# Kernel optimization log

Measured on AMD Instinct MI355X. Metric: run time of the kernel, lower is better.

## Reference

```python
import jax, jax.numpy as jnp
import numpy as np

MARGIN = 0.2  # matches init_kwargs; margin > 0 -> relu hinge branch

N_PARTS, NUM_CLASSES, K_PER_CLASS, D_FEAT = 64, 32, 16, 256


def setup_inputs() -> dict:
    key = jax.random.key(0)
    m = NUM_CLASSES * K_PER_CLASS  # 512
    feature = jax.random.normal(key, (N_PARTS, m, D_FEAT), dtype=jnp.float32)
    # Structured P x K labels: masked_select(...).view(n, m, -1, 1) in the
    # original requires exactly K positives per anchor, so labels must be
    # K samples per class (identical across the part dimension).
    label = jnp.tile(jnp.repeat(jnp.arange(NUM_CLASSES, dtype=jnp.int64), K_PER_CLASS)[None, :], (N_PARTS, 1))
    return {"feature": feature, "label": label, "num_pos": K_PER_CLASS}


def _batch_euc_dist(x):
    # x: [n, m, d] -> dist: [n, m, m]
    x2 = jnp.sum(x * x, axis=2)  # [n, m]
    d2 = x2[:, :, None] + x2[:, None, :] - 2.0 * jnp.einsum('nid,njd->nij', x, x)
    return jnp.sqrt(jax.nn.relu(d2))


def reference(feature, label, num_pos):
    n, m, d = feature.shape
    dist = _batch_euc_dist(feature)  # [n, m, m]
    same = label[:, :, None] == label[:, None, :]  # [n, m, m] bool
    # masked_select preserves flat (row-major) order, so per anchor the
    # selected positives/negatives appear in increasing index order ->
    # stable argsort on the mask reproduces it exactly.
    pos_idx = jnp.argsort(jnp.where(same, 0, 1), axis=-1)[..., :num_pos]        # [n, m, k]
    neg_idx = jnp.argsort(jnp.where(same, 1, 0), axis=-1)[..., :m - num_pos]    # [n, m, m-k]
    hp = jnp.take_along_axis(dist, pos_idx, axis=-1)[:, :, :, None]   # [n, m, k, 1]
    hn = jnp.take_along_axis(dist, neg_idx, axis=-1)[:, :, None, :]   # [n, m, 1, m-k]
    # margin > 0 -> relu hinge (heter/hard/part mining disabled by init flags)
    loss = jax.nn.relu(MARGIN + hp - hn).reshape(n, -1)               # [n, m*k*(m-k)]
    nonzero_num = jnp.sum(loss != 0, axis=1).astype(loss.dtype)       # [n]
    loss_mean = jnp.where(nonzero_num == 0, 0.0,
                          jnp.sum(loss, axis=1) / jnp.maximum(nonzero_num, 1.0))
    return loss_mean.mean(), nonzero_num.mean()
```

## Files before the change

### kernel.cpp

```cpp
#include <hip/hip_runtime.h>
#include <math.h>


#define MARGIN 0.2f
constexpr int NP = 64;
constexpr int M = 512;
constexpr int D = 256;
constexpr int SDS = 20;

typedef __attribute__((ext_vector_type(8))) short bf16x8;
typedef __attribute__((ext_vector_type(4))) float f32x4;

__device__ __forceinline__ unsigned f2bf(float x) {
  unsigned b = __float_as_uint(x);
  return (b + 0x7FFFu + ((b >> 16) & 1u)) >> 16;
}
__device__ __forceinline__ uint4 pack8(float4 v0, float4 v1) {
  uint4 p;
  p.x = f2bf(v0.x) | (f2bf(v0.y) << 16);
  p.y = f2bf(v0.z) | (f2bf(v0.w) << 16);
  p.z = f2bf(v1.x) | (f2bf(v1.y) << 16);
  p.w = f2bf(v1.z) | (f2bf(v1.w) << 16);
  return p;
}

__global__ __launch_bounds__(256, 2) void triplet_kernel(
    const float* __restrict__ feat, float* __restrict__ psum,
    float* __restrict__ pcnt) {
  __shared__ unsigned short As[64 * 32 * 8];
  __shared__ unsigned short Bs[64 * 16 * 8];
  __shared__ float sortd[64 * SDS];
  __shared__ float sumt[64 * SDS];
  __shared__ float x2s[M];
  __shared__ float reds[4], redc[4];

  const int p = blockIdx.y;
  const int diag = blockIdx.x;
  const int i0 = diag * 64;
  const int t = threadIdx.x;
  const int w = t >> 6;
  const int L = t & 63;
  const int tx = L & 15, quad = L >> 4;

  const float* fp = feat + (size_t)p * M * D;

#pragma unroll
  for (int r8 = 0; r8 < 8; r8++) {
    const int row = (t >> 5) + r8 * 8;
    const int c = t & 31;
    const float* src = fp + (size_t)(i0 + row) * D + c * 8;
    float4 v0 = ((const float4*)src)[0];
    float4 v1 = ((const float4*)src)[1];
    *(uint4*)&As[(row * 32 + (c ^ (row & 7))) * 8] = pack8(v0, v1);
  }

  float x2i[4];
  f32x4 srt[4][4];
  float hsum = 0.f;
  int hcnt = 0;

  for (int tt = 0; tt < 8; tt++) {
    const int jt = (diag + tt) & 7;
    const int j0 = jt * 64;
    f32x4 acc[4];
#pragma unroll
    for (int f = 0; f < 4; f++) acc[f] = (f32x4){0.f, 0.f, 0.f, 0.f};
    float rowss[4] = {0.f, 0.f, 0.f, 0.f};

#pragma unroll
    for (int kc = 0; kc < 2; kc++) {
      __syncthreads();
#pragma unroll
      for (int r4 = 0; r4 < 4; r4++) {
        const int row = (t >> 4) + r4 * 16;
        const int c = t & 15;
        const float* src = fp + (size_t)(j0 + row) * D + kc * 128 + c * 8;
        float4 v0 = ((const float4*)src)[0];
        float4 v1 = ((const float4*)src)[1];
        *(uint4*)&Bs[(row * 16 + (c ^ (row & 7))) * 8] = pack8(v0, v1);
        rowss[r4] += v0.x * v0.x + v0.y * v0.y + v0.z * v0.z + v0.w * v0.w +
                     v1.x * v1.x + v1.y * v1.y + v1.z * v1.z + v1.w * v1.w;
      }
      if (kc == 1) {
#pragma unroll
        for (int r4 = 0; r4 < 4; r4++) {
          float ss = rowss[r4];
          ss += __shfl_xor(ss, 8, 16);
          ss += __shfl_xor(ss, 4, 16);
          ss += __shfl_xor(ss, 2, 16);
          ss += __shfl_xor(ss, 1, 16);
          if ((t & 15) == 0) x2s[j0 + (t >> 4) + r4 * 16] = ss;
        }
      }
      __syncthreads();
#pragma unroll
      for (int ks = 0; ks < 4; ks++) {
        const int rowa = w * 16 + tx;
        const int ca = kc * 16 + ks * 4 + quad;
        bf16x8 afrag = *(bf16x8*)&As[(rowa * 32 + (ca ^ (rowa & 7))) * 8];
#pragma unroll
        for (int f = 0; f < 4; f++) {
          const int rowb = f * 16 + tx;
          const int cb = ks * 4 + quad;
          bf16x8 bfrag = *(bf16x8*)&Bs[(rowb * 16 + (cb ^ (rowb & 7))) * 8];
          acc[f] = __builtin_amdgcn_mfma_f32_16x16x32_bf16(afrag, bfrag,
                                                           acc[f], 0, 0, 0);
        }
      }
    }

    if (tt == 0) {
#pragma unroll
      for (int r = 0; r < 4; r++) x2i[r] = x2s[i0 + w * 16 + quad * 4 + r];
      const float xj = x2s[i0 + w * 16 + tx];
#pragma unroll
      for (int r = 0; r < 4; r++) {
        float d2 = x2i[r] + xj - 2.f * acc[w][r];
        sortd[(w * 16 + quad * 4 + r) * SDS + tx] =
            MARGIN + sqrtf(fmaxf(d2, 0.f));
      }
      __syncthreads();
      if (t < 64) {
        float v[16];
#pragma unroll
        for (int q4 = 0; q4 < 4; q4++) {
          f32x4 vv = *(f32x4*)&sortd[t * SDS + q4 * 4];
          v[q4 * 4 + 0] = vv.x; v[q4 * 4 + 1] = vv.y;
          v[q4 * 4 + 2] = vv.z; v[q4 * 4 + 3] = vv.w;
        }
#pragma unroll
        for (int k = 2; k <= 16; k <<= 1)
#pragma unroll
          for (int j = k >> 1; j > 0; j >>= 1)
#pragma unroll
            for (int i = 0; i < 16; i++) {
              const int l = i ^ j;
              if (l > i) {
                const bool asc = ((i & k) == 0);
                if (asc ? (v[i] > v[l]) : (v[i] < v[l])) {
                  float tmp = v[i]; v[i] = v[l]; v[l] = tmp;
                }
              }
            }
#pragma unroll
        for (int q4 = 0; q4 < 4; q4++)
          *(f32x4*)&sortd[t * SDS + q4 * 4] =
              (f32x4){v[q4 * 4], v[q4 * 4 + 1], v[q4 * 4 + 2], v[q4 * 4 + 3]};
        float run = 0.f;
        sumt[t * SDS + 0] = 0.f;
#pragma unroll
        for (int c = 1; c <= 16; c++) {
          run += v[16 - c];
          sumt[t * SDS + c] = run;
        }
      }
      __syncthreads();
#pragma unroll
      for (int r = 0; r < 4; r++)
#pragma unroll
        for (int q4 = 0; q4 < 4; q4++)
          srt[r][q4] = *(f32x4*)&sortd[(w * 16 + quad * 4 + r) * SDS + q4 * 4];
    }

#pragma unroll
    for (int f = 0; f < 4; f++) {
      if (tt == 0 && f == w) continue;
      const float xj = x2s[j0 + f * 16 + tx];
#pragma unroll
      for (int r = 0; r < 4; r++) {
        const float dn = sqrtf(fmaxf(x2i[r] + xj - 2.f * acc[f][r], 0.f));
        int c = 0;
#define CMP(sv) c += ((sv) > dn) ? 1 : 0;
        CMP(srt[r][0].x) CMP(srt[r][0].y) CMP(srt[r][0].z) CMP(srt[r][0].w)
        CMP(srt[r][1].x) CMP(srt[r][1].y) CMP(srt[r][1].z) CMP(srt[r][1].w)
        CMP(srt[r][2].x) CMP(srt[r][2].y) CMP(srt[r][2].z) CMP(srt[r][2].w)
        CMP(srt[r][3].x) CMP(srt[r][3].y) CMP(srt[r][3].z) CMP(srt[r][3].w)
#undef CMP
        const float stv = sumt[(w * 16 + quad * 4 + r) * SDS + c];
        hsum += stv;
        hsum = fmaf(-(float)c, dn, hsum);
        hcnt += c;
      }
    }
  }

  float cf = (float)hcnt;
  for (int off = 32; off > 0; off >>= 1) {
    hsum += __shfl_down(hsum, off, 64);
    cf += __shfl_down(cf, off, 64);
  }
  if (L == 0) { reds[w] = hsum; redc[w] = cf; }
  __syncthreads();
  if (t == 0) {
    psum[p * 8 + diag] = reds[0] + reds[1] + reds[2] + reds[3];
    pcnt[p * 8 + diag] = redc[0] + redc[1] + redc[2] + redc[3];
  }
}

__global__ __launch_bounds__(64) void finalize_kernel(
    const float* __restrict__ psum, const float* __restrict__ pcnt,
    float* __restrict__ out) {
  const int p = threadIdx.x;
  float s = 0.f, c = 0.f;
#pragma unroll
  for (int tt = 0; tt < 8; tt++) {
    s += psum[p * 8 + tt];
    c += pcnt[p * 8 + tt];
  }
  float lm = (c == 0.f) ? 0.f : s / fmaxf(c, 1.f);
  float ctot = c;
  for (int off = 32; off > 0; off >>= 1) {
    lm += __shfl_down(lm, off, 64);
    ctot += __shfl_down(ctot, off, 64);
  }
  if (p == 0) {
    out[0] = lm / 64.f;
    out[1] = ctot / 64.f;
  }
}

extern "C" void kernel_launch(void* const* d_in, const int* in_sizes, int n_in,
                              void* d_out, int out_size, void* d_ws,
                              size_t ws_size, hipStream_t stream) {
  const float* feat = (const float*)d_in[0];
  float* ws = (float*)d_ws;
  float* psum = ws;
  float* pcnt = ws + 512;
  float* out = (float*)d_out;

  dim3 grid(8, NP);
  triplet_kernel<<<grid, 256, 0, stream>>>(feat, psum, pcnt);
  finalize_kernel<<<1, 64, 0, stream>>>(psum, pcnt, out);
}
```

Before: 134.4 us.

## Prefetch next B tile into registers, peel diagonal tile to reuse A tile, swap grid axes

```diff
diff --git a/kernel.cpp b/kernel.cpp
--- a/kernel.cpp
+++ b/kernel.cpp
@@ -23,19 +23,23 @@
   p.w = f2bf(v1.z) | (f2bf(v1.w) << 16);
   return p;
 }
+__device__ __forceinline__ float sq8(float4 v0, float4 v1) {
+  return v0.x * v0.x + v0.y * v0.y + v0.z * v0.z + v0.w * v0.w +
+         v1.x * v1.x + v1.y * v1.y + v1.z * v1.z + v1.w * v1.w;
+}
 
 __global__ __launch_bounds__(256, 2) void triplet_kernel(
     const float* __restrict__ feat, float* __restrict__ psum,
     float* __restrict__ pcnt) {
   __shared__ unsigned short As[64 * 32 * 8];
-  __shared__ unsigned short Bs[64 * 16 * 8];
+  __shared__ unsigned short Bs[2][64 * 16 * 8];
   __shared__ float sortd[64 * SDS];
   __shared__ float sumt[64 * SDS];
   __shared__ float x2s[M];
   __shared__ float reds[4], redc[4];
 
-  const int p = blockIdx.y;
-  const int diag = blockIdx.x;
+  const int p = blockIdx.x;
+  const int diag = blockIdx.y;
   const int i0 = diag * 64;
   const int t = threadIdx.x;
   const int w = t >> 6;
@@ -43,6 +47,20 @@
   const int tx = L & 15, quad = L >> 4;
 
   const float* fp = feat + (size_t)p * M * D;
+
+  const int br = t >> 4, bc = t & 15;
+
+  float4 R[8];
+  {
+    const int nj0 = ((diag + 1) & 7) * 64;
+    const float* s0 = fp + (size_t)(nj0 + br) * D + bc * 8;
+#pragma unroll
+    for (int r4 = 0; r4 < 4; r4++) {
+      const float* src = s0 + (size_t)(r4 * 16) * D;
+      R[r4 * 2] = ((const float4*)src)[0];
+      R[r4 * 2 + 1] = ((const float4*)src)[1];
+    }
+  }
 
 #pragma unroll
   for (int r8 = 0; r8 < 8; r8++) {
@@ -52,34 +70,129 @@
     float4 v0 = ((const float4*)src)[0];
     float4 v1 = ((const float4*)src)[1];
     *(uint4*)&As[(row * 32 + (c ^ (row & 7))) * 8] = pack8(v0, v1);
-  }
+    float ss = sq8(v0, v1);
+    ss += __shfl_xor(ss, 16, 32);
+    ss += __shfl_xor(ss, 8, 32);
+    ss += __shfl_xor(ss, 4, 32);
+    ss += __shfl_xor(ss, 2, 32);
+    ss += __shfl_xor(ss, 1, 32);
+    if ((t & 31) == 0) x2s[i0 + row] = ss;
+  }
+  __syncthreads();
 
   float x2i[4];
   f32x4 srt[4][4];
   float hsum = 0.f;
   int hcnt = 0;
-
-  for (int tt = 0; tt < 8; tt++) {
-    const int jt = (diag + tt) & 7;
-    const int j0 = jt * 64;
+  float rowss[4];
+
+  {
     f32x4 acc[4];
 #pragma unroll
     for (int f = 0; f < 4; f++) acc[f] = (f32x4){0.f, 0.f, 0.f, 0.f};
-    float rowss[4] = {0.f, 0.f, 0.f, 0.f};
+#pragma unroll
+    for (int kc = 0; kc < 2; kc++)
+#pragma unroll
+      for (int ks = 0; ks < 4; ks++) {
+        const int rowa = w * 16 + tx;
+        const int ca = kc * 16 + ks * 4 + quad;
+        bf16x8 afrag = *(bf16x8*)&As[(rowa * 32 + (ca ^ (rowa & 7))) * 8];
+#pragma unroll
+        for (int f = 0; f < 4; f++) {
+          const int rowb = f * 16 + tx;
+          bf16x8 bfrag = *(bf16x8*)&As[(rowb * 32 + (ca ^ (rowb & 7))) * 8];
+          acc[f] = __builtin_amdgcn_mfma_f32_16x16x32_bf16(afrag, bfrag,
+                                                           acc[f], 0, 0, 0);
+        }
+      }
+#pragma unroll
+    for (int r = 0; r < 4; r++) x2i[r] = x2s[i0 + w * 16 + quad * 4 + r];
+    const float xj = x2s[i0 + w * 16 + tx];
+#pragma unroll
+    for (int r = 0; r < 4; r++) {
+      float d2 = x2i[r] + xj - 2.f * acc[w][r];
+      sortd[(w * 16 + quad * 4 + r) * SDS + tx] =
+          MARGIN + sqrtf(fmaxf(d2, 0.f));
+    }
+    __syncthreads();
+    if (t < 64) {
+      float v[16];
+#pragma unroll
+      for (int q4 = 0; q4 < 4; q4++) {
+        f32x4 vv = *(f32x4*)&sortd[t * SDS + q4 * 4];
+        v[q4 * 4 + 0] = vv.x; v[q4 * 4 + 1] = vv.y;
+        v[q4 * 4 + 2] = vv.z; v[q4 * 4 + 3] = vv.w;
+      }
+#pragma unroll
+      for (int k = 2; k <= 16; k <<= 1)
+#pragma unroll
+        for (int j = k >> 1; j > 0; j >>= 1)
+#pragma unroll
+          for (int i = 0; i < 16; i++) {
+            const int l = i ^ j;
+            if (l > i) {
+              const bool asc = ((i & k) == 0);
+              if (asc ? (v[i] > v[l]) : (v[i] < v[l])) {
+                float tmp = v[i]; v[i] = v[l]; v[l] = tmp;
+              }
+            }
+          }
+#pragma unroll
+      for (int q4 = 0; q4 < 4; q4++)
+        *(f32x4*)&sortd[t * SDS + q4 * 4] =
+            (f32x4){v[q4 * 4], v[q4 * 4 + 1], v[q4 * 4 + 2], v[q4 * 4 + 3]};
+      float run = 0.f;
+      sumt[t * SDS + 0] = 0.f;
+#pragma unroll
+      for (int c = 1; c <= 16; c++) {
+        run += v[16 - c];
+        sumt[t * SDS + c] = run;
+      }
+    }
+    __syncthreads();
+#pragma unroll
+    for (int r = 0; r < 4; r++)
+#pragma unroll
+      for (int q4 = 0; q4 < 4; q4++)
+        srt[r][q4] = *(f32x4*)&sortd[(w * 16 + quad * 4 + r) * SDS + q4 * 4];
+
+#pragma unroll
+    for (int f = 0; f < 4; f++) {
+      if (f == w) continue;
+      const float xj2 = x2s[i0 + f * 16 + tx];
+#pragma unroll
+      for (int r = 0; r < 4; r++) {
+        const float dn = sqrtf(fmaxf(x2i[r] + xj2 - 2.f * acc[f][r], 0.f));
+        int c = 0;
+#define CMP(sv) c += ((sv) > dn) ? 1 : 0;
+        CMP(srt[r][0].x) CMP(srt[r][0].y) CMP(srt[r][0].z) CMP(srt[r][0].w)
+        CMP(srt[r][1].x) CMP(srt[r][1].y) CMP(srt[r][1].z) CMP(srt[r][1].w)
+        CMP(srt[r][2].x) CMP(srt[r][2].y) CMP(srt[r][2].z) CMP(srt[r][2].w)
+        CMP(srt[r][3].x) CMP(srt[r][3].y) CMP(srt[r][3].z) CMP(srt[r][3].w)
+#undef CMP
+        hsum += sumt[(w * 16 + quad * 4 + r) * SDS + c];
+        hsum = fmaf(-(float)c, dn, hsum);
+        hcnt += c;
+      }
+    }
+  }
+
+  for (int tt = 1; tt < 8; tt++) {
+    const int j0 = ((diag + tt) & 7) * 64;
+    f32x4 acc[4];
+#pragma unroll
+    for (int f = 0; f < 4; f++) acc[f] = (f32x4){0.f, 0.f, 0.f, 0.f};
 
 #pragma unroll
     for (int kc = 0; kc < 2; kc++) {
       __syncthreads();
 #pragma unroll
       for (int r4 = 0; r4 < 4; r4++) {
-        const int row = (t >> 4) + r4 * 16;
-        const int c = t & 15;
-        const float* src = fp + (size_t)(j0 + row) * D + kc * 128 + c * 8;
-        float4 v0 = ((const float4*)src)[0];
-        float4 v1 = ((const float4*)src)[1];
-        *(uint4*)&Bs[(row * 16 + (c ^ (row & 7))) * 8] = pack8(v0, v1);
-        rowss[r4] += v0.x * v0.x + v0.y * v0.y + v0.z * v0.z + v0.w * v0.w +
-                     v1.x * v1.x + v1.y * v1.y + v1.z * v1.z + v1.w * v1.w;
+        const int row = br + r4 * 16;
+        float4 v0 = R[r4 * 2], v1 = R[r4 * 2 + 1];
+        *(uint4*)&Bs[kc][(row * 16 + (bc ^ (row & 7))) * 8] = pack8(v0, v1);
+        const float s8 = sq8(v0, v1);
+        rowss[r4] = (kc == 0) ? s8 : rowss[r4] + s8;
       }
       if (kc == 1) {
 #pragma unroll
@@ -89,7 +202,19 @@
           ss += __shfl_xor(ss, 4, 16);
           ss += __shfl_xor(ss, 2, 16);
           ss += __shfl_xor(ss, 1, 16);
-          if ((t & 15) == 0) x2s[j0 + (t >> 4) + r4 * 16] = ss;
+          if (bc == 0) x2s[j0 + br + r4 * 16] = ss;
+        }
+      }
+      const int ntt = (kc == 0) ? tt : tt + 1;
+      if (ntt < 8) {
+        const int nkc = kc ^ 1;
+        const int nj0 = ((diag + ntt) & 7) * 64;
+        const float* s0 = fp + (size_t)(nj0 + br) * D + nkc * 128 + bc * 8;
+#pragma unroll
+        for (int r4 = 0; r4 < 4; r4++) {
+          const float* src = s0 + (size_t)(r4 * 16) * D;
+          R[r4 * 2] = ((const float4*)src)[0];
+          R[r4 * 2 + 1] = ((const float4*)src)[1];
         }
       }
       __syncthreads();
@@ -102,69 +227,15 @@
         for (int f = 0; f < 4; f++) {
           const int rowb = f * 16 + tx;
           const int cb = ks * 4 + quad;
-          bf16x8 bfrag = *(bf16x8*)&Bs[(rowb * 16 + (cb ^ (rowb & 7))) * 8];
+          bf16x8 bfrag = *(bf16x8*)&Bs[kc][(rowb * 16 + (cb ^ (rowb & 7))) * 8];
           acc[f] = __builtin_amdgcn_mfma_f32_16x16x32_bf16(afrag, bfrag,
                                                            acc[f], 0, 0, 0);
         }
       }
     }
 
-    if (tt == 0) {
-#pragma unroll
-      for (int r = 0; r < 4; r++) x2i[r] = x2s[i0 + w * 16 + quad * 4 + r];
-      const float xj = x2s[i0 + w * 16 + tx];
-#pragma unroll
-      for (int r = 0; r < 4; r++) {
-        float d2 = x2i[r] + xj - 2.f * acc[w][r];
-        sortd[(w * 16 + quad * 4 + r) * SDS + tx] =
-            MARGIN + sqrtf(fmaxf(d2, 0.f));
-      }
-      __syncthreads();
-      if (t < 64) {
-        float v[16];
-#pragma unroll
-        for (int q4 = 0; q4 < 4; q4++) {
-          f32x4 vv = *(f32x4*)&sortd[t * SDS + q4 * 4];
-          v[q4 * 4 + 0] = vv.x; v[q4 * 4 + 1] = vv.y;
-          v[q4 * 4 + 2] = vv.z; v[q4 * 4 + 3] = vv.w;
-        }
-#pragma unroll
-        for (int k = 2; k <= 16; k <<= 1)
-#pragma unroll
-          for (int j = k >> 1; j > 0; j >>= 1)
-#pragma unroll
-            for (int i = 0; i < 16; i++) {
-              const int l = i ^ j;
-              if (l > i) {
-                const bool asc = ((i & k) == 0);
-                if (asc ? (v[i] > v[l]) : (v[i] < v[l])) {
-                  float tmp = v[i]; v[i] = v[l]; v[l] = tmp;
-                }
-              }
-            }
-#pragma unroll
-        for (int q4 = 0; q4 < 4; q4++)
-          *(f32x4*)&sortd[t * SDS + q4 * 4] =
-              (f32x4){v[q4 * 4], v[q4 * 4 + 1], v[q4 * 4 + 2], v[q4 * 4 + 3]};
-        float run = 0.f;
-        sumt[t * SDS + 0] = 0.f;
-#pragma unroll
-        for (int c = 1; c <= 16; c++) {
-          run += v[16 - c];
-          sumt[t * SDS + c] = run;
-        }
-      }
-      __syncthreads();
-#pragma unroll
-      for (int r = 0; r < 4; r++)
-#pragma unroll
-        for (int q4 = 0; q4 < 4; q4++)
-          srt[r][q4] = *(f32x4*)&sortd[(w * 16 + quad * 4 + r) * SDS + q4 * 4];
-    }
-
 #pragma unroll
     for (int f = 0; f < 4; f++) {
-      if (tt == 0 && f == w) continue;
       const float xj = x2s[j0 + f * 16 + tx];
 #pragma unroll
       for (int r = 0; r < 4; r++) {
@@ -176,8 +247,7 @@
         CMP(srt[r][2].x) CMP(srt[r][2].y) CMP(srt[r][2].z) CMP(srt[r][2].w)
         CMP(srt[r][3].x) CMP(srt[r][3].y) CMP(srt[r][3].z) CMP(srt[r][3].w)
 #undef CMP
-        const float stv = sumt[(w * 16 + quad * 4 + r) * SDS + c];
-        hsum += stv;
+        hsum += sumt[(w * 16 + quad * 4 + r) * SDS + c];
         hsum = fmaf(-(float)c, dn, hsum);
         hcnt += c;
       }
@@ -228,7 +298,7 @@
   float* pcnt = ws + 512;
   float* out = (float*)d_out;
 
-  dim3 grid(8, NP);
+  dim3 grid(NP, 8);
   triplet_kernel<<<grid, 256, 0, stream>>>(feat, psum, pcnt);
   finalize_kernel<<<1, 64, 0, stream>>>(psum, pcnt, out);
 }
```

Result: faster. 125.0 us (-7.0%).

## Split anchor tiles across two blocks and keep A fragments in registers

Applied to the files above, without the earlier changes.

```diff
diff --git a/kernel.cpp b/kernel.cpp
--- a/kernel.cpp
+++ b/kernel.cpp
@@ -15,7 +15,7 @@
   unsigned b = __float_as_uint(x);
   return (b + 0x7FFFu + ((b >> 16) & 1u)) >> 16;
 }
-__device__ __forceinline__ uint4 pack8(float4 v0, float4 v1) {
+__device__ __forceinline__ uint4 pack8u(float4 v0, float4 v1) {
   uint4 p;
   p.x = f2bf(v0.x) | (f2bf(v0.y) << 16);
   p.y = f2bf(v0.z) | (f2bf(v0.w) << 16);
@@ -23,63 +23,71 @@
   p.w = f2bf(v1.z) | (f2bf(v1.w) << 16);
   return p;
 }
-
-__global__ __launch_bounds__(256, 2) void triplet_kernel(
+__device__ __forceinline__ bf16x8 pack8b(float4 v0, float4 v1) {
+  union { uint4 u; bf16x8 b; } cv;
+  cv.u = pack8u(v0, v1);
+  return cv.b;
+}
+__device__ __forceinline__ float sq8(float4 v0, float4 v1) {
+  return v0.x * v0.x + v0.y * v0.y + v0.z * v0.z + v0.w * v0.w +
+         v1.x * v1.x + v1.y * v1.y + v1.z * v1.z + v1.w * v1.w;
+}
+
+__global__ __launch_bounds__(256, 3) void triplet_kernel(
     const float* __restrict__ feat, float* __restrict__ psum,
     float* __restrict__ pcnt) {
-  __shared__ unsigned short As[64 * 32 * 8];
   __shared__ unsigned short Bs[64 * 16 * 8];
   __shared__ float sortd[64 * SDS];
   __shared__ float sumt[64 * SDS];
-  __shared__ float x2s[M];
+  __shared__ float x2s[64];
   __shared__ float reds[4], redc[4];
 
-  const int p = blockIdx.y;
-  const int diag = blockIdx.x;
+  const int p = blockIdx.x;
+  const int diag = blockIdx.y;
+  const int h = blockIdx.z;
   const int i0 = diag * 64;
   const int t = threadIdx.x;
-  const int w = t >> 6;
-  const int L = t & 63;
+  const int w = t >> 6, L = t & 63;
   const int tx = L & 15, quad = L >> 4;
+  const int br = t >> 4, bc = t & 15;
 
   const float* fp = feat + (size_t)p * M * D;
 
-#pragma unroll
-  for (int r8 = 0; r8 < 8; r8++) {
-    const int row = (t >> 5) + r8 * 8;
-    const int c = t & 31;
-    const float* src = fp + (size_t)(i0 + row) * D + c * 8;
-    float4 v0 = ((const float4*)src)[0];
-    float4 v1 = ((const float4*)src)[1];
-    *(uint4*)&As[(row * 32 + (c ^ (row & 7))) * 8] = pack8(v0, v1);
-  }
+  bf16x8 af[8];
+#pragma unroll
+  for (int kc = 0; kc < 2; kc++)
+#pragma unroll
+    for (int ks = 0; ks < 4; ks++) {
+      const float* src =
+          fp + (size_t)(i0 + w * 16 + tx) * D + kc * 128 + (ks * 4 + quad) * 8;
+      af[kc * 4 + ks] = pack8b(((const float4*)src)[0], ((const float4*)src)[1]);
+    }
 
   float x2i[4];
   f32x4 srt[4][4];
   float hsum = 0.f;
   int hcnt = 0;
 
-  for (int tt = 0; tt < 8; tt++) {
-    const int jt = (diag + tt) & 7;
-    const int j0 = jt * 64;
+  const int ntiles = 4 + h;
+  for (int ti = 0; ti < ntiles; ti++) {
+    const int tt = (ti == 0) ? 0 : ti + h * 3;
+    const int j0 = ((diag + tt) & 7) * 64;
     f32x4 acc[4];
 #pragma unroll
     for (int f = 0; f < 4; f++) acc[f] = (f32x4){0.f, 0.f, 0.f, 0.f};
-    float rowss[4] = {0.f, 0.f, 0.f, 0.f};
+    float rowss[4];
 
 #pragma unroll
     for (int kc = 0; kc < 2; kc++) {
       __syncthreads();
 #pragma unroll
       for (int r4 = 0; r4 < 4; r4++) {
-        const int row = (t >> 4) + r4 * 16;
-        const int c = t & 15;
-        const float* src = fp + (size_t)(j0 + row) * D + kc * 128 + c * 8;
-        float4 v0 = ((const float4*)src)[0];
-        float4 v1 = ((const float4*)src)[1];
-        *(uint4*)&Bs[(row * 16 + (c ^ (row & 7))) * 8] = pack8(v0, v1);
-        rowss[r4] += v0.x * v0.x + v0.y * v0.y + v0.z * v0.z + v0.w * v0.w +
-                     v1.x * v1.x + v1.y * v1.y + v1.z * v1.z + v1.w * v1.w;
+        const int row = br + r4 * 16;
+        const float* src = fp + (size_t)(j0 + row) * D + kc * 128 + bc * 8;
+        float4 v0 = ((const float4*)src)[0], v1 = ((const float4*)src)[1];
+        *(uint4*)&Bs[(row * 16 + (bc ^ (row & 7))) * 8] = pack8u(v0, v1);
+        const float s8 = sq8(v0, v1);
+        rowss[r4] = kc ? rowss[r4] + s8 : s8;
       }
       if (kc == 1) {
 #pragma unroll
@@ -89,30 +97,27 @@
           ss += __shfl_xor(ss, 4, 16);
           ss += __shfl_xor(ss, 2, 16);
           ss += __shfl_xor(ss, 1, 16);
-          if ((t & 15) == 0) x2s[j0 + (t >> 4) + r4 * 16] = ss;
+          if (bc == 0) x2s[br + r4 * 16] = ss;
         }
       }
       __syncthreads();
 #pragma unroll
       for (int ks = 0; ks < 4; ks++) {
-        const int rowa = w * 16 + tx;
-        const int ca = kc * 16 + ks * 4 + quad;
-        bf16x8 afrag = *(bf16x8*)&As[(rowa * 32 + (ca ^ (rowa & 7))) * 8];
+        const bf16x8 a = af[kc * 4 + ks];
 #pragma unroll
         for (int f = 0; f < 4; f++) {
-          const int rowb = f * 16 + tx;
-          const int cb = ks * 4 + quad;
-          bf16x8 bfrag = *(bf16x8*)&Bs[(rowb * 16 + (cb ^ (rowb & 7))) * 8];
-          acc[f] = __builtin_amdgcn_mfma_f32_16x16x32_bf16(afrag, bfrag,
-                                                           acc[f], 0, 0, 0);
+          const int rowb = f * 16 + tx, cb = ks * 4 + quad;
+          bf16x8 b = *(bf16x8*)&Bs[(rowb * 16 + (cb ^ (rowb & 7))) * 8];
+          acc[f] =
+              __builtin_amdgcn_mfma_f32_16x16x32_bf16(a, b, acc[f], 0, 0, 0);
         }
       }
     }
 
-    if (tt == 0) {
-#pragma unroll
-      for (int r = 0; r < 4; r++) x2i[r] = x2s[i0 + w * 16 + quad * 4 + r];
-      const float xj = x2s[i0 + w * 16 + tx];
+    if (ti == 0) {
+#pragma unroll
+      for (int r = 0; r < 4; r++) x2i[r] = x2s[w * 16 + quad * 4 + r];
+      const float xj = x2s[w * 16 + tx];
 #pragma unroll
       for (int r = 0; r < 4; r++) {
         float d2 = x2i[r] + xj - 2.f * acc[w][r];
@@ -160,26 +165,46 @@
 #pragma unroll
         for (int q4 = 0; q4 < 4; q4++)
           srt[r][q4] = *(f32x4*)&sortd[(w * 16 + quad * 4 + r) * SDS + q4 * 4];
-    }
-
-#pragma unroll
-    for (int f = 0; f < 4; f++) {
-      if (tt == 0 && f == w) continue;
-      const float xj = x2s[j0 + f * 16 + tx];
-#pragma unroll
-      for (int r = 0; r < 4; r++) {
-        const float dn = sqrtf(fmaxf(x2i[r] + xj - 2.f * acc[f][r], 0.f));
-        int c = 0;
+
+      if (h == 0) {
+#pragma unroll
+        for (int f = 0; f < 4; f++) {
+          if (f == w) continue;
+          const float xj2 = x2s[f * 16 + tx];
+#pragma unroll
+          for (int r = 0; r < 4; r++) {
+            const float dn = sqrtf(fmaxf(x2i[r] + xj2 - 2.f * acc[f][r], 0.f));
+            int c = 0;
 #define CMP(sv) c += ((sv) > dn) ? 1 : 0;
-        CMP(srt[r][0].x) CMP(srt[r][0].y) CMP(srt[r][0].z) CMP(srt[r][0].w)
-        CMP(srt[r][1].x) CMP(srt[r][1].y) CMP(srt[r][1].z) CMP(srt[r][1].w)
-        CMP(srt[r][2].x) CMP(srt[r][2].y) CMP(srt[r][2].z) CMP(srt[r][2].w)
-        CMP(srt[r][3].x) CMP(srt[r][3].y) CMP(srt[r][3].z) CMP(srt[r][3].w)
+            CMP(srt[r][0].x) CMP(srt[r][0].y) CMP(srt[r][0].z) CMP(srt[r][0].w)
+            CMP(srt[r][1].x) CMP(srt[r][1].y) CMP(srt[r][1].z) CMP(srt[r][1].w)
+            CMP(srt[r][2].x) CMP(srt[r][2].y) CMP(srt[r][2].z) CMP(srt[r][2].w)
+            CMP(srt[r][3].x) CMP(srt[r][3].y) CMP(srt[r][3].z) CMP(srt[r][3].w)
 #undef CMP
-        const float stv = sumt[(w * 16 + quad * 4 + r) * SDS + c];
-        hsum += stv;
-        hsum = fmaf(-(float)c, dn, hsum);
-        hcnt += c;
+            hsum += sumt[(w * 16 + quad * 4 + r) * SDS + c];
+            hsum = fmaf(-(float)c, dn, hsum);
+            hcnt += c;
+          }
+        }
+      }
+    } else {
+#pragma unroll
+      for (int f = 0; f < 4; f++) {
+        const float xj = x2s[f * 16 + tx];
+#pragma unroll
+        for (int r = 0; r < 4; r++) {
+          const float dn = sqrtf(fmaxf(x2i[r] + xj - 2.f * acc[f][r], 0.f));
+          int c = 0;
+#define CMP(sv) c += ((sv) > dn) ? 1 : 0;
+          CMP(srt[r][0].x) CMP(srt[r][0].y) CMP(srt[r][0].z) CMP(srt[r][0].w)
+          CMP(srt[r][1].x) CMP(srt[r][1].y) CMP(srt[r][1].z) CMP(srt[r][1].w)
+          CMP(srt[r][2].x) CMP(srt[r][2].y) CMP(srt[r][2].z) CMP(srt[r][2].w)
+          CMP(srt[r][3].x) CMP(srt[r][3].y) CMP(srt[r][3].z) CMP(srt[r][3].w)
+#undef CMP
+          hsum += sumt[(w * 16 + quad * 4 + r) * SDS + c];
+          hsum = fmaf(-(float)c, dn, hsum);
+          hcnt += c;
+        }
       }
     }
   }
@@ -192,8 +217,8 @@
   if (L == 0) { reds[w] = hsum; redc[w] = cf; }
   __syncthreads();
   if (t == 0) {
-    psum[p * 8 + diag] = reds[0] + reds[1] + reds[2] + reds[3];
-    pcnt[p * 8 + diag] = redc[0] + redc[1] + redc[2] + redc[3];
+    psum[p * 16 + diag * 2 + h] = reds[0] + reds[1] + reds[2] + reds[3];
+    pcnt[p * 16 + diag * 2 + h] = redc[0] + redc[1] + redc[2] + redc[3];
   }
 }
 
@@ -203,9 +228,9 @@
   const int p = threadIdx.x;
   float s = 0.f, c = 0.f;
 #pragma unroll
-  for (int tt = 0; tt < 8; tt++) {
-    s += psum[p * 8 + tt];
-    c += pcnt[p * 8 + tt];
+  for (int i = 0; i < 16; i++) {
+    s += psum[p * 16 + i];
+    c += pcnt[p * 16 + i];
   }
   float lm = (c == 0.f) ? 0.f : s / fmaxf(c, 1.f);
   float ctot = c;
@@ -225,10 +250,10 @@
   const float* feat = (const float*)d_in[0];
   float* ws = (float*)d_ws;
   float* psum = ws;
-  float* pcnt = ws + 512;
+  float* pcnt = ws + 1024;
   float* out = (float*)d_out;
 
-  dim3 grid(8, NP);
+  dim3 grid(NP, 8, 2);
   triplet_kernel<<<grid, 256, 0, stream>>>(feat, psum, pcnt);
   finalize_kernel<<<1, 64, 0, stream>>>(psum, pcnt, out);
 }
```

Result: slower. 195.9 us (+45.8%).
